# Performance work log

Hardware: AMD Instinct MI355X
Metric: run time of the kernel (lower is better)

The kernel has to match this reference:

```python
import jax, jax.numpy as jnp
import numpy as np

B, T, C, NH = 4, 2048, 1024, 16
HS = C // NH


def setup_inputs() -> dict:
    key = jax.random.key(0)
    k1, k2, k3, k4, k5 = jax.random.split(key, 5)
    s = 1.0 / np.sqrt(C)
    return {
        "x": jax.random.normal(k1, (B, T, C), dtype=jnp.float32),
        "Wqkv": jax.random.normal(k2, (3 * C, C), dtype=jnp.float32) * s,
        "bqkv": jax.random.normal(k3, (3 * C,), dtype=jnp.float32) * 0.02,
        "Wproj": jax.random.normal(k4, (C, C), dtype=jnp.float32) * s,
        "bproj": jax.random.normal(k5, (C,), dtype=jnp.float32) * 0.02,
    }


def reference(x, Wqkv, bqkv, Wproj, bproj):
    Bsz, Tlen, Cdim = x.shape
    # qkv projection (torch Linear: x @ W.T + b)
    qkv = x @ Wqkv.T + bqkv                      # [B, T, 3C]
    q, k, v = jnp.split(qkv, 3, axis=-1)
    # [B, NH, T, HS]
    q = q.reshape(Bsz, Tlen, NH, HS).transpose(0, 2, 1, 3)
    k = k.reshape(Bsz, Tlen, NH, HS).transpose(0, 2, 1, 3)
    v = v.reshape(Bsz, Tlen, NH, HS).transpose(0, 2, 1, 3)
    scale = 1.0 / np.sqrt(HS)
    att = jnp.einsum('bhqd,bhkd->bhqk', q, k) * scale
    causal = jnp.triu(jnp.ones((Tlen, Tlen), dtype=bool), k=1)
    att = jnp.where(causal[None, None], -jnp.inf, att)
    att = jax.nn.softmax(att, axis=-1)
    y = jnp.einsum('bhqk,bhkd->bhqd', att, v)    # [B, NH, T, HS]
    y = y.transpose(0, 2, 1, 3).reshape(Bsz, Tlen, Cdim)
    return y @ Wproj.T + bproj
```

## Files before the change

kernel.cpp:

```cpp
#include <hip/hip_runtime.h>
#include <hip/hip_bf16.h>

#define B_   4
#define T_   2048
#define C_   1024
#define NH_  16
#define HS_  64
#define M_   8192
#define N1_  3072
#define BH_  64

typedef __attribute__((ext_vector_type(8))) short short8;
typedef __attribute__((ext_vector_type(4))) short short4v;
typedef __attribute__((ext_vector_type(4))) float f32x4;

__device__ __forceinline__ short f2bf(float f) {
  unsigned u = __float_as_uint(f);
  unsigned r = (u + 0x7fffu + ((u >> 16) & 1u)) >> 16;
  return (short)r;
}
__device__ __forceinline__ unsigned pk_bf16(float a, float b) {
  __hip_bfloat162 h = __float22bfloat162_rn(make_float2(a, b));
  union { __hip_bfloat162 h2; unsigned u; } cv; cv.h2 = h; return cv.u;
}

typedef __attribute__((address_space(1))) unsigned int as1_uint;
typedef __attribute__((address_space(3))) unsigned int as3_uint;
__device__ __forceinline__ void g2l16(const void* g, void* l) {
  __builtin_amdgcn_global_load_lds((as1_uint*)g, (as3_uint*)l, 16, 0, 0);
}

__global__ __launch_bounds__(256) void conv_bf16(
    const float* __restrict__ src, short* __restrict__ dst)
{
  const size_t i = ((size_t)blockIdx.x * 256 + threadIdx.x) * 8;
  const f32x4 a = *(const f32x4*)&src[i];
  const f32x4 b = *(const f32x4*)&src[i + 4];
  short8 o;
  o[0] = f2bf(a[0]); o[1] = f2bf(a[1]); o[2] = f2bf(a[2]); o[3] = f2bf(a[3]);
  o[4] = f2bf(b[0]); o[5] = f2bf(b[1]); o[6] = f2bf(b[2]); o[7] = f2bf(b[3]);
  *(short8*)&dst[i] = o;
}

__global__ __launch_bounds__(256) void qkv_gemm(
    const short* __restrict__ X,
    const short* __restrict__ W,
    const float* __restrict__ bias,
    short* __restrict__ Qo, short* __restrict__ Ko, short* __restrict__ Vt)
{
  __shared__ short As[128 * 32];
  __shared__ short Bs[128 * 32];
  const int tid = threadIdx.x;
  const int lane = tid & 63;
  const int wid = tid >> 6;
  const int wy = wid >> 1, wx = wid & 1;
  const int lq = lane >> 4, lm = lane & 15;
  const int row0 = blockIdx.x * 128;
  const int col0 = blockIdx.y * 128;

  f32x4 acc[4][4] = {};

  const int c0 = tid, c1 = tid + 256;
  const int ar0 = c0 >> 2, ak0 = (c0 & 3) << 3;
  const int ar1 = c1 >> 2, ak1 = (c1 & 3) << 3;

  for (int k0 = 0; k0 < C_; k0 += 32) {
    __syncthreads();
    g2l16(&X[(size_t)(row0 + ar0) * C_ + k0 + ak0], &As[c0 * 8]);
    g2l16(&X[(size_t)(row0 + ar1) * C_ + k0 + ak1], &As[c1 * 8]);
    g2l16(&W[(size_t)(col0 + ar0) * C_ + k0 + ak0], &Bs[c0 * 8]);
    g2l16(&W[(size_t)(col0 + ar1) * C_ + k0 + ak1], &Bs[c1 * 8]);
    __syncthreads();

    short8 af[4], bfr[4];
#pragma unroll
    for (int mi = 0; mi < 4; ++mi)
      af[mi] = *(const short8*)&As[(wy * 64 + mi * 16 + lm) * 32 + lq * 8];
#pragma unroll
    for (int ni = 0; ni < 4; ++ni)
      bfr[ni] = *(const short8*)&Bs[(wx * 64 + ni * 16 + lm) * 32 + lq * 8];
#pragma unroll
    for (int mi = 0; mi < 4; ++mi)
#pragma unroll
      for (int ni = 0; ni < 4; ++ni)
        acc[mi][ni] = __builtin_amdgcn_mfma_f32_16x16x32_bf16(af[mi], bfr[ni], acc[mi][ni], 0, 0, 0);
  }

#pragma unroll
  for (int ni = 0; ni < 4; ++ni) {
    const int n = col0 + wx * 64 + ni * 16 + lm;
    const float bv = bias[n];
    const int sel = n >> 10;
    const int cc = n & (C_ - 1);
    const int h = cc >> 6, d = cc & 63;
    if (sel == 2) {
#pragma unroll
      for (int mi = 0; mi < 4; ++mi) {
        const int m0 = row0 + wy * 64 + mi * 16 + lq * 4;
        const int b = m0 >> 11, t0 = m0 & (T_ - 1);
        const int bh = b * NH_ + h;
        short4v o;
#pragma unroll
        for (int i = 0; i < 4; ++i) o[i] = f2bf(acc[mi][ni][i] + bv);
        *(short4v*)&Vt[((size_t)bh * HS_ + d) * T_ + t0] = o;
      }
    } else {
      short* dst = (sel == 0) ? Qo : Ko;
#pragma unroll
      for (int mi = 0; mi < 4; ++mi) {
#pragma unroll
        for (int i = 0; i < 4; ++i) {
          const int m = row0 + wy * 64 + mi * 16 + lq * 4 + i;
          const int b = m >> 11, t = m & (T_ - 1);
          const int bh = b * NH_ + h;
          dst[((size_t)bh * T_ + t) * HS_ + d] = f2bf(acc[mi][ni][i] + bv);
        }
      }
    }
  }
}

__global__ __launch_bounds__(256) void proj_gemm(
    const short* __restrict__ Y,
    const short* __restrict__ W,
    const float* __restrict__ bias,
    float* __restrict__ Out)
{
  __shared__ short As[128 * 32];
  __shared__ short Bs[128 * 32];
  const int tid = threadIdx.x;
  const int lane = tid & 63;
  const int wid = tid >> 6;
  const int wy = wid >> 1, wx = wid & 1;
  const int lq = lane >> 4, lm = lane & 15;
  const int row0 = blockIdx.x * 128;
  const int col0 = blockIdx.y * 128;

  f32x4 acc[4][4] = {};

  const int c0 = tid, c1 = tid + 256;
  const int ar0 = c0 >> 2, ak0 = (c0 & 3) << 3;
  const int ar1 = c1 >> 2, ak1 = (c1 & 3) << 3;

  for (int k0 = 0; k0 < C_; k0 += 32) {
    __syncthreads();
    g2l16(&Y[(size_t)(row0 + ar0) * C_ + k0 + ak0], &As[c0 * 8]);
    g2l16(&Y[(size_t)(row0 + ar1) * C_ + k0 + ak1], &As[c1 * 8]);
    g2l16(&W[(size_t)(col0 + ar0) * C_ + k0 + ak0], &Bs[c0 * 8]);
    g2l16(&W[(size_t)(col0 + ar1) * C_ + k0 + ak1], &Bs[c1 * 8]);
    __syncthreads();

    short8 af[4], bfr[4];
#pragma unroll
    for (int mi = 0; mi < 4; ++mi)
      af[mi] = *(const short8*)&As[(wy * 64 + mi * 16 + lm) * 32 + lq * 8];
#pragma unroll
    for (int ni = 0; ni < 4; ++ni)
      bfr[ni] = *(const short8*)&Bs[(wx * 64 + ni * 16 + lm) * 32 + lq * 8];
#pragma unroll
    for (int mi = 0; mi < 4; ++mi)
#pragma unroll
      for (int ni = 0; ni < 4; ++ni)
        acc[mi][ni] = __builtin_amdgcn_mfma_f32_16x16x32_bf16(af[mi], bfr[ni], acc[mi][ni], 0, 0, 0);
  }

#pragma unroll
  for (int ni = 0; ni < 4; ++ni) {
    const int n = col0 + wx * 64 + ni * 16 + lm;
    const float bv = bias[n];
#pragma unroll
    for (int mi = 0; mi < 4; ++mi) {
#pragma unroll
      for (int i = 0; i < 4; ++i) {
        const int m = row0 + wy * 64 + mi * 16 + lq * 4 + i;
        Out[(size_t)m * C_ + n] = acc[mi][ni][i] + bv;
      }
    }
  }
}

#define LDK 72
__global__ __launch_bounds__(256) void attn(
    const short* __restrict__ Qg, const short* __restrict__ Kg,
    const short* __restrict__ Vg, short* __restrict__ Yo)
{
  __shared__ short Ks[64 * LDK];
  __shared__ short Vs[64 * LDK];

  const int tid = threadIdx.x;
  const int lane = tid & 63;
  const int w = tid >> 6;
  const int lq = lane >> 4, lm = lane & 15;
  const int bh = blockIdx.y;
  const int b = bh >> 4, h = bh & 15;
  const size_t base = (size_t)bh * T_ * HS_;
  const short* __restrict__ Kb = Kg + base;
  const short* __restrict__ Vb = Vg + base;
  const float sf = 0.125f * 1.44269504089f;

  const int sr = tid >> 3;
  const int sc = (tid & 7) * 8;

#pragma unroll 1
  for (int half = 0; half < 2; ++half) {
    const int qt = half ? (int)blockIdx.x : 31 - (int)blockIdx.x;
    const int q0 = qt * 64;
    const int q = q0 + w * 16 + lm;

    const short8 qf0 = *(const short8*)&Qg[base + (size_t)q * HS_ + lq * 8];
    const short8 qf1 = *(const short8*)&Qg[base + (size_t)q * HS_ + 32 + lq * 8];

    float m_run = -3.0e38f, l_run = 0.0f;
    f32x4 o_acc[4] = {};

    short8 pk0 = *(const short8*)&Kb[(size_t)sr * HS_ + sc];
    short8 pk1 = *(const short8*)&Kb[(size_t)(32 + sr) * HS_ + sc];
    short8 pv0 = *(const short8*)&Vb[(size_t)sr * T_ + sc];
    short8 pv1 = *(const short8*)&Vb[(size_t)(32 + sr) * T_ + sc];

#pragma unroll 1
    for (int kt = 0; kt <= qt; ++kt) {
      const int kv0 = kt * 64;

      __syncthreads();
      *(short8*)&Ks[sr * LDK + sc] = pk0;
      *(short8*)&Ks[(32 + sr) * LDK + sc] = pk1;
      *(short8*)&Vs[sr * LDK + sc] = pv0;
      *(short8*)&Vs[(32 + sr) * LDK + sc] = pv1;
      __syncthreads();

      if (kt < qt) {
        const int nk = kv0 + 64;
        pk0 = *(const short8*)&Kb[(size_t)(nk + sr) * HS_ + sc];
        pk1 = *(const short8*)&Kb[(size_t)(nk + 32 + sr) * HS_ + sc];
        pv0 = *(const short8*)&Vb[(size_t)sr * T_ + nk + sc];
        pv1 = *(const short8*)&Vb[(size_t)(32 + sr) * T_ + nk + sc];
      }

      f32x4 sv[4];
#pragma unroll
      for (int ni = 0; ni < 4; ++ni) {
        const short8 kf0 = *(const short8*)&Ks[(ni * 16 + lm) * LDK + lq * 8];
        const short8 kf1 = *(const short8*)&Ks[(ni * 16 + lm) * LDK + 32 + lq * 8];
        f32x4 s = {};
        s = __builtin_amdgcn_mfma_f32_16x16x32_bf16(kf0, qf0, s, 0, 0, 0);
        sv[ni] = __builtin_amdgcn_mfma_f32_16x16x32_bf16(kf1, qf1, s, 0, 0, 0);
      }

      if (kt == qt) {
#pragma unroll
        for (int ni = 0; ni < 4; ++ni) {
          const int kvb = kv0 + ni * 16 + lq * 4;
#pragma unroll
          for (int i = 0; i < 4; ++i)
            if (kvb + i > q) sv[ni][i] = -3.0e38f;
        }
      }

      float v = fmaxf(fmaxf(fmaxf(sv[0][0], sv[0][1]), fmaxf(sv[0][2], sv[0][3])),
                      fmaxf(fmaxf(sv[1][0], sv[1][1]), fmaxf(sv[1][2], sv[1][3])));
      v = fmaxf(v, fmaxf(fmaxf(fmaxf(sv[2][0], sv[2][1]), fmaxf(sv[2][2], sv[2][3])),
                         fmaxf(fmaxf(sv[3][0], sv[3][1]), fmaxf(sv[3][2], sv[3][3]))));
      v = fmaxf(v, __shfl_xor(v, 16));
      v = fmaxf(v, __shfl_xor(v, 32));
      const float mnew = fmaxf(m_run, v);
      const float alpha = __builtin_amdgcn_exp2f((m_run - mnew) * sf);
      const float nb = -mnew * sf;
      m_run = mnew;

#pragma unroll
      for (int ni = 0; ni < 4; ++ni)
#pragma unroll
        for (int i = 0; i < 4; ++i)
          sv[ni][i] = __builtin_amdgcn_exp2f(__builtin_fmaf(sv[ni][i], sf, nb));

      float s = ((sv[0][0] + sv[0][1]) + (sv[0][2] + sv[0][3]))
              + ((sv[1][0] + sv[1][1]) + (sv[1][2] + sv[1][3]))
              + ((sv[2][0] + sv[2][1]) + (sv[2][2] + sv[2][3]))
              + ((sv[3][0] + sv[3][1]) + (sv[3][2] + sv[3][3]));
      s += __shfl_xor(s, 16);
      s += __shfl_xor(s, 32);
      l_run = l_run * alpha + s;

#pragma unroll
      for (int di = 0; di < 4; ++di)
#pragma unroll
        for (int i = 0; i < 4; ++i)
          o_acc[di][i] *= alpha;

      short4v p4[4];
#pragma unroll
      for (int ni = 0; ni < 4; ++ni) {
        union { short4v s4; unsigned u[2]; } pk;
        pk.u[0] = pk_bf16(sv[ni][0], sv[ni][1]);
        pk.u[1] = pk_bf16(sv[ni][2], sv[ni][3]);
        p4[ni] = pk.s4;
      }

#pragma unroll
      for (int di = 0; di < 4; ++di) {
#pragma unroll
        for (int ni = 0; ni < 4; ++ni) {
          const short4v vfr = *(const short4v*)&Vs[(di * 16 + lm) * LDK + ni * 16 + lq * 4];
          o_acc[di] = __builtin_amdgcn_mfma_f32_16x16x16bf16_1k(vfr, p4[ni], o_acc[di], 0, 0, 0);
        }
      }
    }

    const float rl = 1.0f / l_run;
    const size_t rowo = ((size_t)(b * T_ + q)) * C_ + h * HS_;
#pragma unroll
    for (int di = 0; di < 4; ++di) {
      union { short4v s4; unsigned u[2]; } pk;
      pk.u[0] = pk_bf16(o_acc[di][0] * rl, o_acc[di][1] * rl);
      pk.u[1] = pk_bf16(o_acc[di][2] * rl, o_acc[di][3] * rl);
      *(short4v*)&Yo[rowo + di * 16 + lq * 4] = pk.s4;
    }
  }
}

extern "C" void kernel_launch(void* const* d_in, const int* in_sizes, int n_in,
                              void* d_out, int out_size, void* d_ws, size_t ws_size,
                              hipStream_t stream) {
  (void)in_sizes; (void)n_in; (void)out_size;
  const float* x     = (const float*)d_in[0];
  const float* Wqkv  = (const float*)d_in[1];
  const float* bqkv  = (const float*)d_in[2];
  const float* Wproj = (const float*)d_in[3];
  const float* bproj = (const float*)d_in[4];
  float* out = (float*)d_out;

  const size_t nWq = (size_t)N1_ * C_;
  const size_t nWp = (size_t)C_ * C_;
  const size_t nFull = (size_t)M_ * C_;
  const size_t nB = (size_t)T_ * C_;

  dim3 blk(256);
  const size_t need_batched = (nWq + nWp + 4 * nFull) * sizeof(short);

  if (ws_size >= need_batched) {
    short* Wq_bf = (short*)d_ws;
    short* Wp_bf = Wq_bf + nWq;
    short* S0    = Wp_bf + nWp;
    short* Qw    = S0 + nFull;
    short* Kw    = Qw + nFull;
    short* Vw    = Kw + nFull;

    conv_bf16<<<dim3((int)(nWq / 2048)), blk, 0, stream>>>(Wqkv, Wq_bf);
    conv_bf16<<<dim3((int)(nWp / 2048)), blk, 0, stream>>>(Wproj, Wp_bf);
    conv_bf16<<<dim3((int)(nFull / 2048)), blk, 0, stream>>>(x, S0);
    qkv_gemm<<<dim3(M_ / 128, N1_ / 128), blk, 0, stream>>>(S0, Wq_bf, bqkv, Qw, Kw, Vw);
    attn<<<dim3(16, BH_), blk, 0, stream>>>(Qw, Kw, Vw, S0);
    proj_gemm<<<dim3(M_ / 128, C_ / 128), blk, 0, stream>>>(S0, Wp_bf, bproj, out);
  } else {
    short* Wq_bf = (short*)d_ws;
    short* Wp_bf = Wq_bf + nWq;
    short* S0    = Wp_bf + nWp;
    short* Qw    = S0 + nB;
    short* Kw    = Qw + nB;
    short* Vw    = Kw + nB;

    conv_bf16<<<dim3((int)(nWq / 2048)), blk, 0, stream>>>(Wqkv, Wq_bf);
    conv_bf16<<<dim3((int)(nWp / 2048)), blk, 0, stream>>>(Wproj, Wp_bf);
    for (int b = 0; b < B_; ++b) {
      const float* xb = x   + (size_t)b * nB;
      float*       ob = out + (size_t)b * nB;
      conv_bf16<<<dim3((int)(nB / 2048)), blk, 0, stream>>>(xb, S0);
      qkv_gemm<<<dim3(T_ / 128, N1_ / 128), blk, 0, stream>>>(S0, Wq_bf, bqkv, Qw, Kw, Vw);
      attn<<<dim3(16, NH_), blk, 0, stream>>>(Qw, Kw, Vw, S0);
      proj_gemm<<<dim3(T_ / 128, C_ / 128), blk, 0, stream>>>(S0, Wp_bf, bproj, ob);
    }
  }
}
```

Before: 276.6 us.

## Deepen GEMM K-tile, swap MFMA operands for vector stores, reorder attention grid

Both GEMMs now stage a 64-wide K slice per barrier instead of 32, which halves the number of sync rounds and doubles LDS use. The MFMA operand order is swapped for Q/K and the output projection, so each lane holds four consecutive columns. That allows vectorized bias loads and 8-byte bf16 or 16-byte fp32 stores in place of scalar scattered stores. The attention grid is flattened to 1D with the head index varying fastest, which changes the order in which causal-balanced tiles are dispatched across CUs.

```diff
diff --git a/kernel.cpp b/kernel.cpp
--- a/kernel.cpp
+++ b/kernel.cpp
@@ -48,8 +48,8 @@
     const float* __restrict__ bias,
     short* __restrict__ Qo, short* __restrict__ Ko, short* __restrict__ Vt)
 {
-  __shared__ short As[128 * 32];
-  __shared__ short Bs[128 * 32];
+  __shared__ short As[128 * 64];
+  __shared__ short Bs[128 * 64];
   const int tid = threadIdx.x;
   const int lane = tid & 63;
   const int wid = tid >> 6;
@@ -57,43 +57,73 @@
   const int lq = lane >> 4, lm = lane & 15;
   const int row0 = blockIdx.x * 128;
   const int col0 = blockIdx.y * 128;
+  const int sel = col0 >> 10;
 
   f32x4 acc[4][4] = {};
 
-  const int c0 = tid, c1 = tid + 256;
-  const int ar0 = c0 >> 2, ak0 = (c0 & 3) << 3;
-  const int ar1 = c1 >> 2, ak1 = (c1 & 3) << 3;
-
-  for (int k0 = 0; k0 < C_; k0 += 32) {
+  const int r = tid >> 3;
+  const int cc = (tid & 7) * 8;
+
+  for (int k0 = 0; k0 < C_; k0 += 64) {
     __syncthreads();
-    g2l16(&X[(size_t)(row0 + ar0) * C_ + k0 + ak0], &As[c0 * 8]);
-    g2l16(&X[(size_t)(row0 + ar1) * C_ + k0 + ak1], &As[c1 * 8]);
-    g2l16(&W[(size_t)(col0 + ar0) * C_ + k0 + ak0], &Bs[c0 * 8]);
-    g2l16(&W[(size_t)(col0 + ar1) * C_ + k0 + ak1], &Bs[c1 * 8]);
+#pragma unroll
+    for (int j = 0; j < 4; ++j) {
+      g2l16(&X[(size_t)(row0 + r + 32 * j) * C_ + k0 + cc], &As[tid * 8 + 2048 * j]);
+      g2l16(&W[(size_t)(col0 + r + 32 * j) * C_ + k0 + cc], &Bs[tid * 8 + 2048 * j]);
+    }
     __syncthreads();
 
-    short8 af[4], bfr[4];
-#pragma unroll
-    for (int mi = 0; mi < 4; ++mi)
-      af[mi] = *(const short8*)&As[(wy * 64 + mi * 16 + lm) * 32 + lq * 8];
-#pragma unroll
-    for (int ni = 0; ni < 4; ++ni)
-      bfr[ni] = *(const short8*)&Bs[(wx * 64 + ni * 16 + lm) * 32 + lq * 8];
-#pragma unroll
-    for (int mi = 0; mi < 4; ++mi)
+#pragma unroll
+    for (int kk = 0; kk < 2; ++kk) {
+      short8 af[4], bfr[4];
+#pragma unroll
+      for (int mi = 0; mi < 4; ++mi)
+        af[mi] = *(const short8*)&As[(wy * 64 + mi * 16 + lm) * 64 + kk * 32 + lq * 8];
 #pragma unroll
       for (int ni = 0; ni < 4; ++ni)
-        acc[mi][ni] = __builtin_amdgcn_mfma_f32_16x16x32_bf16(af[mi], bfr[ni], acc[mi][ni], 0, 0, 0);
-  }
-
-#pragma unroll
-  for (int ni = 0; ni < 4; ++ni) {
-    const int n = col0 + wx * 64 + ni * 16 + lm;
-    const float bv = bias[n];
-    const int sel = n >> 10;
-    const int cc = n & (C_ - 1);
-    const int h = cc >> 6, d = cc & 63;
-    if (sel == 2) {
+        bfr[ni] = *(const short8*)&Bs[(wx * 64 + ni * 16 + lm) * 64 + kk * 32 + lq * 8];
+      if (sel < 2) {
+#pragma unroll
+        for (int mi = 0; mi < 4; ++mi)
+#pragma unroll
+          for (int ni = 0; ni < 4; ++ni)
+            acc[mi][ni] = __builtin_amdgcn_mfma_f32_16x16x32_bf16(bfr[ni], af[mi], acc[mi][ni], 0, 0, 0);
+      } else {
+#pragma unroll
+        for (int mi = 0; mi < 4; ++mi)
+#pragma unroll
+          for (int ni = 0; ni < 4; ++ni)
+            acc[mi][ni] = __builtin_amdgcn_mfma_f32_16x16x32_bf16(af[mi], bfr[ni], acc[mi][ni], 0, 0, 0);
+      }
+    }
+  }
+
+  if (sel < 2) {
+    short* dst = (sel == 0) ? Qo : Ko;
+#pragma unroll
+    for (int ni = 0; ni < 4; ++ni) {
+      const int n0 = col0 + wx * 64 + ni * 16 + lq * 4;
+      const f32x4 bv4 = *(const f32x4*)&bias[n0];
+      const int cc0 = n0 & (C_ - 1);
+      const int h = cc0 >> 6, d0 = cc0 & 63;
+#pragma unroll
+      for (int mi = 0; mi < 4; ++mi) {
+        const int m = row0 + wy * 64 + mi * 16 + lm;
+        const int b = m >> 11, t = m & (T_ - 1);
+        const int bh = b * NH_ + h;
+        short4v o;
+#pragma unroll
+        for (int i = 0; i < 4; ++i) o[i] = f2bf(acc[mi][ni][i] + bv4[i]);
+        *(short4v*)&dst[((size_t)(bh * T_ + t)) * HS_ + d0] = o;
+      }
+    }
+  } else {
+#pragma unroll
+    for (int ni = 0; ni < 4; ++ni) {
+      const int n = col0 + wx * 64 + ni * 16 + lm;
+      const float bv = bias[n];
+      const int ccn = n & (C_ - 1);
+      const int h = ccn >> 6, d = ccn & 63;
 #pragma unroll
       for (int mi = 0; mi < 4; ++mi) {
         const int m0 = row0 + wy * 64 + mi * 16 + lq * 4;
@@ -103,18 +133,6 @@
 #pragma unroll
         for (int i = 0; i < 4; ++i) o[i] = f2bf(acc[mi][ni][i] + bv);
         *(short4v*)&Vt[((size_t)bh * HS_ + d) * T_ + t0] = o;
-      }
-    } else {
-      short* dst = (sel == 0) ? Qo : Ko;
-#pragma unroll
-      for (int mi = 0; mi < 4; ++mi) {
-#pragma unroll
-        for (int i = 0; i < 4; ++i) {
-          const int m = row0 + wy * 64 + mi * 16 + lq * 4 + i;
-          const int b = m >> 11, t = m & (T_ - 1);
-          const int bh = b * NH_ + h;
-          dst[((size_t)bh * T_ + t) * HS_ + d] = f2bf(acc[mi][ni][i] + bv);
-        }
       }
     }
   }
@@ -126,8 +144,8 @@
     const float* __restrict__ bias,
     float* __restrict__ Out)
 {
-  __shared__ short As[128 * 32];
-  __shared__ short Bs[128 * 32];
+  __shared__ short As[128 * 64];
+  __shared__ short Bs[128 * 64];
   const int tid = threadIdx.x;
   const int lane = tid & 63;
   const int wid = tid >> 6;
@@ -138,48 +156,50 @@
 
   f32x4 acc[4][4] = {};
 
-  const int c0 = tid, c1 = tid + 256;
-  const int ar0 = c0 >> 2, ak0 = (c0 & 3) << 3;
-  const int ar1 = c1 >> 2, ak1 = (c1 & 3) << 3;
-
-  for (int k0 = 0; k0 < C_; k0 += 32) {
+  const int r = tid >> 3;
+  const int cc = (tid & 7) * 8;
+
+  for (int k0 = 0; k0 < C_; k0 += 64) {
     __syncthreads();
-    g2l16(&Y[(size_t)(row0 + ar0) * C_ + k0 + ak0], &As[c0 * 8]);
-    g2l16(&Y[(size_t)(row0 + ar1) * C_ + k0 + ak1], &As[c1 * 8]);
-    g2l16(&W[(size_t)(col0 + ar0) * C_ + k0 + ak0], &Bs[c0 * 8]);
-    g2l16(&W[(size_t)(col0 + ar1) * C_ + k0 + ak1], &Bs[c1 * 8]);
+#pragma unroll
+    for (int j = 0; j < 4; ++j) {
+      g2l16(&Y[(size_t)(row0 + r + 32 * j) * C_ + k0 + cc], &As[tid * 8 + 2048 * j]);
+      g2l16(&W[(size_t)(col0 + r + 32 * j) * C_ + k0 + cc], &Bs[tid * 8 + 2048 * j]);
+    }
     __syncthreads();
 
-    short8 af[4], bfr[4];
-#pragma unroll
-    for (int mi = 0; mi < 4; ++mi)
-      af[mi] = *(const short8*)&As[(wy * 64 + mi * 16 + lm) * 32 + lq * 8];
-#pragma unroll
-    for (int ni = 0; ni < 4; ++ni)
-      bfr[ni] = *(const short8*)&Bs[(wx * 64 + ni * 16 + lm) * 32 + lq * 8];
-#pragma unroll
-    for (int mi = 0; mi < 4; ++mi)
+#pragma unroll
+    for (int kk = 0; kk < 2; ++kk) {
+      short8 af[4], bfr[4];
+#pragma unroll
+      for (int mi = 0; mi < 4; ++mi)
+        af[mi] = *(const short8*)&As[(wy * 64 + mi * 16 + lm) * 64 + kk * 32 + lq * 8];
 #pragma unroll
       for (int ni = 0; ni < 4; ++ni)
-        acc[mi][ni] = __builtin_amdgcn_mfma_f32_16x16x32_bf16(af[mi], bfr[ni], acc[mi][ni], 0, 0, 0);
+        bfr[ni] = *(const short8*)&Bs[(wx * 64 + ni * 16 + lm) * 64 + kk * 32 + lq * 8];
+#pragma unroll
+      for (int mi = 0; mi < 4; ++mi)
+#pragma unroll
+        for (int ni = 0; ni < 4; ++ni)
+          acc[mi][ni] = __builtin_amdgcn_mfma_f32_16x16x32_bf16(bfr[ni], af[mi], acc[mi][ni], 0, 0, 0);
+    }
   }
 
 #pragma unroll
   for (int ni = 0; ni < 4; ++ni) {
-    const int n = col0 + wx * 64 + ni * 16 + lm;
-    const float bv = bias[n];
+    const int n0 = col0 + wx * 64 + ni * 16 + lq * 4;
+    const f32x4 bv4 = *(const f32x4*)&bias[n0];
 #pragma unroll
     for (int mi = 0; mi < 4; ++mi) {
-#pragma unroll
-      for (int i = 0; i < 4; ++i) {
-        const int m = row0 + wy * 64 + mi * 16 + lq * 4 + i;
-        Out[(size_t)m * C_ + n] = acc[mi][ni][i] + bv;
-      }
+      const int m = row0 + wy * 64 + mi * 16 + lm;
+      f32x4 o = acc[mi][ni] + bv4;
+      *(f32x4*)&Out[(size_t)m * C_ + n0] = o;
     }
   }
 }
 
 #define LDK 72
+template <int NBH>
 __global__ __launch_bounds__(256) void attn(
     const short* __restrict__ Qg, const short* __restrict__ Kg,
     const short* __restrict__ Vg, short* __restrict__ Yo)
@@ -191,7 +211,9 @@
   const int lane = tid & 63;
   const int w = tid >> 6;
   const int lq = lane >> 4, lm = lane & 15;
-  const int bh = blockIdx.y;
+  const int id = blockIdx.x;
+  const int bh = id & (NBH - 1);
+  const int kblk = id / NBH;
   const int b = bh >> 4, h = bh & 15;
   const size_t base = (size_t)bh * T_ * HS_;
   const short* __restrict__ Kb = Kg + base;
@@ -203,7 +225,7 @@
 
 #pragma unroll 1
   for (int half = 0; half < 2; ++half) {
-    const int qt = half ? (int)blockIdx.x : 31 - (int)blockIdx.x;
+    const int qt = half ? kblk : 31 - kblk;
     const int q0 = qt * 64;
     const int q = q0 + w * 16 + lm;
 
@@ -350,7 +372,7 @@
     conv_bf16<<<dim3((int)(nWp / 2048)), blk, 0, stream>>>(Wproj, Wp_bf);
     conv_bf16<<<dim3((int)(nFull / 2048)), blk, 0, stream>>>(x, S0);
     qkv_gemm<<<dim3(M_ / 128, N1_ / 128), blk, 0, stream>>>(S0, Wq_bf, bqkv, Qw, Kw, Vw);
-    attn<<<dim3(16, BH_), blk, 0, stream>>>(Qw, Kw, Vw, S0);
+    attn<BH_><<<dim3(16 * BH_), blk, 0, stream>>>(Qw, Kw, Vw, S0);
     proj_gemm<<<dim3(M_ / 128, C_ / 128), blk, 0, stream>>>(S0, Wp_bf, bproj, out);
   } else {
     short* Wq_bf = (short*)d_ws;
@@ -367,7 +389,7 @@
       float*       ob = out + (size_t)b * nB;
       conv_bf16<<<dim3((int)(nB / 2048)), blk, 0, stream>>>(xb, S0);
       qkv_gemm<<<dim3(T_ / 128, N1_ / 128), blk, 0, stream>>>(S0, Wq_bf, bqkv, Qw, Kw, Vw);
-      attn<<<dim3(16, NH_), blk, 0, stream>>>(Qw, Kw, Vw, S0);
+      attn<NH_><<<dim3(16 * NH_), blk, 0, stream>>>(Qw, Kw, Vw, S0);
       proj_gemm<<<dim3(T_ / 128, C_ / 128), blk, 0, stream>>>(S0, Wp_bf, bproj, ob);
     }
   }
```

Measured after the change: 282.6 us. +2.2%, slower.
